# Kernel tuning notes

Measured on AMD Instinct MI355X. Metric: run time of the kernel, lower is better.

Reference implementation:

```python
import jax, jax.numpy as jnp
import numpy as np

B, T, D = 2, 2048, 1024
H = 16
HD = D // H
WINDOW = 128
N_GLOBAL = 1
SCALE = 1.0 / np.sqrt(HD)


def _attend_mask(T):
    # True = allowed to attend: banded local window + global rows/cols
    idx = jnp.arange(T)
    dist = jnp.abs(idx[:, None] - idx[None, :])
    attend = dist <= WINDOW
    glb = idx < N_GLOBAL
    attend = attend | glb[:, None] | glb[None, :]
    return attend  # [T, T] bool


def setup_inputs() -> dict:
    key = jax.random.key(0)
    ks = jax.random.split(key, 5)
    scale_w = 1.0 / np.sqrt(D)
    return {
        "x": jax.random.normal(ks[0], (B, T, D), dtype=jnp.float32),
        "Wq": jax.random.normal(ks[1], (D, D), dtype=jnp.float32) * scale_w,
        "Wk": jax.random.normal(ks[2], (D, D), dtype=jnp.float32) * scale_w,
        "Wv": jax.random.normal(ks[3], (D, D), dtype=jnp.float32) * scale_w,
        "Wo": jax.random.normal(ks[4], (D, D), dtype=jnp.float32) * scale_w,
    }


def reference(x, Wq, Wk, Wv, Wo):
    Bb, Tt, Dd = x.shape
    # torch nn.Linear: y = x @ W.T
    q = (x @ Wq.T).reshape(Bb, Tt, H, HD).transpose(0, 2, 1, 3)  # [B,H,T,hd]
    k = (x @ Wk.T).reshape(Bb, Tt, H, HD).transpose(0, 2, 1, 3)
    v = (x @ Wv.T).reshape(Bb, Tt, H, HD).transpose(0, 2, 1, 3)

    attend = _attend_mask(Tt)  # [T,T]
    logits = jnp.einsum("bhqd,bhkd->bhqk", q, k) * SCALE
    logits = jnp.where(attend[None, None, :, :], logits, -jnp.inf)
    weights = jax.nn.softmax(logits, axis=-1)
    weights = jnp.nan_to_num(weights)
    out = jnp.einsum("bhqk,bhkd->bhqd", weights, v)
    out = out.transpose(0, 2, 1, 3).reshape(Bb, Tt, Dd)
    return out @ Wo.T
```

## Files before the change

kernel.cpp:

```cpp
#include <hip/hip_runtime.h>

typedef unsigned short u16;
typedef __attribute__((ext_vector_type(8))) __bf16 bf16x8;
typedef __attribute__((ext_vector_type(4))) float f32x4;
typedef __attribute__((ext_vector_type(8))) u16 u16x8;

#define T_SEQ 2048
#define DIM   1024
#define HDIM  64
#define WIN   128
#define XN_EL (2 * T_SEQ * DIM)
#define VP    392

#define AS1 __attribute__((address_space(1)))
#define AS3 __attribute__((address_space(3)))

__device__ __forceinline__ u16 f2bf(float f) {
  union { float f; unsigned u; } v; v.f = f;
  unsigned r = v.u + 0x7fffu + ((v.u >> 16) & 1u);
  return (u16)(r >> 16);
}
__device__ __forceinline__ float bf2f(u16 u) {
  union { unsigned u; float f; } v; v.u = ((unsigned)u) << 16; return v.f;
}
__device__ __forceinline__ void bar() {
  asm volatile("" ::: "memory");
  __builtin_amdgcn_s_barrier();
  asm volatile("" ::: "memory");
}

__global__ __launch_bounds__(256) void cvt_all(
    const float* __restrict__ x,  const float* __restrict__ wq,
    const float* __restrict__ wk, const float* __restrict__ wv,
    const float* __restrict__ wo, u16* __restrict__ xb, u16* __restrict__ wb) {
  const int bid = blockIdx.x;
  const float* s;
  u16* d;
  int off;
  if (bid < 2048) {
    s = x; d = xb; off = bid * 2048;
  } else {
    const int w = bid - 2048;
    const int m = w >> 9;
    s = (m == 0) ? wq : ((m == 1) ? wk : ((m == 2) ? wv : wo));
    d = wb + ((size_t)m << 20);
    off = (w & 511) * 2048;
  }
  const int i = off + threadIdx.x * 8;
  const float4* s4 = (const float4*)(s + i);
  float4 a = s4[0], b = s4[1];
  u16x8 r;
  r[0] = f2bf(a.x); r[1] = f2bf(a.y); r[2] = f2bf(a.z); r[3] = f2bf(a.w);
  r[4] = f2bf(b.x); r[5] = f2bf(b.y); r[6] = f2bf(b.z); r[7] = f2bf(b.w);
  *(u16x8*)(d + i) = r;
}

__global__ __launch_bounds__(512, 2) void gemm8(
    const u16* __restrict__ A, const u16* __restrict__ B,
    u16* __restrict__ C, int nbm) {
  constexpr int NT = 16;
  __shared__ u16 As[2][256 * 64];
  __shared__ u16 Bs[2][192 * 64];

  const int tid = threadIdx.x;
  const int lane = tid & 63;
  const int wid = tid >> 6;
  const int wr = wid >> 2, wc = wid & 3;
  const int c15 = lane & 15, g = lane >> 4;
  const int lr = lane >> 3;
  const int lcs = ((lane & 7) ^ lr) << 3;

  const int cpx = gridDim.x >> 3;
  const int bid = ((int)blockIdx.x & 7) * cpx + ((int)blockIdx.x >> 3);
  const int bm = bid % nbm;
  const int nb = bid / nbm;
  const u16* Ab = A + (size_t)bm * 256 * DIM;
  const u16* Bb = B + (size_t)nb * 192 * DIM;

  f32x4 acc[8][3];
#pragma unroll
  for (int m = 0; m < 8; ++m)
#pragma unroll
    for (int n = 0; n < 3; ++n) acc[m][n] = (f32x4){0.f, 0.f, 0.f, 0.f};

  auto stAh = [&](int buf, int half, int t) {
    const int k0 = t * 64;
#pragma unroll
    for (int i = 0; i < 2; ++i) {
      const int c = half * 16 + wid * 2 + i;
      __builtin_amdgcn_global_load_lds(
          (const AS1 void*)(Ab + (size_t)(c * 8 + lr) * DIM + k0 + lcs),
          (AS3 void*)(&As[buf][c * 512]), 16, 0, 0);
    }
  };
  auto stBt = [&](int buf, int third, int t) {
    const int k0 = t * 64;
    const int c = third * 8 + wid;
    __builtin_amdgcn_global_load_lds(
        (const AS1 void*)(Bb + (size_t)(c * 8 + lr) * DIM + k0 + lcs),
        (AS3 void*)(&Bs[buf][c * 512]), 16, 0, 0);
  };

  stAh(0, 0, 0); stAh(0, 1, 0);
  stBt(0, 0, 0); stBt(0, 1, 0); stBt(0, 2, 0);
  stBt(1, 0, 1); stBt(1, 1, 1); stBt(1, 2, 1);
  asm volatile("s_waitcnt vmcnt(3)" ::: "memory");
  bar();

  for (int t2 = 0; t2 < NT; t2 += 2) {
    bf16x8 bfrag[3][2];
#pragma unroll
    for (int p = 0; p < 8; ++p) {
      const int q = p & 3;
      const int buf = (p >> 2);
      if (q == 0) {
#pragma unroll
        for (int n = 0; n < 3; ++n)
#pragma unroll
          for (int ks = 0; ks < 2; ++ks) {
            const int r = wc * 48 + n * 16 + c15;
            bfrag[n][ks] = *(const bf16x8*)(
                &Bs[buf][r * 64 + ((ks * 32 + g * 8) ^ ((r & 7) << 3))]);
          }
      }
      bf16x8 af[2][2];
#pragma unroll
      for (int m = 0; m < 2; ++m)
#pragma unroll
        for (int ks = 0; ks < 2; ++ks) {
          const int r = wr * 128 + (q * 2 + m) * 16 + c15;
          af[m][ks] = *(const bf16x8*)(
              &As[buf][r * 64 + ((ks * 32 + g * 8) ^ ((r & 7) << 3))]);
        }
      const bool s2 = (t2 + 2) < NT;
      const bool s3 = (t2 + 3) < NT;
      if (p == 0) {
        stAh(1, 0, t2 + 1);
      } else if (p == 1) {
        stAh(1, 1, t2 + 1);
        if (s2) stBt(0, 0, t2 + 2);
      } else if (p == 2) {
        if (s2) stBt(0, 1, t2 + 2);
      } else if (p == 3) {
        if (s2) { stBt(0, 2, t2 + 2);
                  asm volatile("s_waitcnt vmcnt(3)" ::: "memory"); }
        else    { asm volatile("s_waitcnt vmcnt(0)" ::: "memory"); }
      } else if (p == 4) {
        if (s2) stAh(0, 0, t2 + 2);
      } else if (p == 5) {
        if (s2) stAh(0, 1, t2 + 2);
        if (s3) stBt(1, 0, t2 + 3);
      } else if (p == 6) {
        if (s3) stBt(1, 1, t2 + 3);
      } else {
        if (s3) { stBt(1, 2, t2 + 3);
                  asm volatile("s_waitcnt vmcnt(3)" ::: "memory"); }
        else if (s2) { asm volatile("s_waitcnt vmcnt(0)" ::: "memory"); }
      }
      bar();
      __builtin_amdgcn_s_setprio(1);
#pragma unroll
      for (int m = 0; m < 2; ++m)
#pragma unroll
        for (int n = 0; n < 3; ++n)
#pragma unroll
          for (int ks = 0; ks < 2; ++ks)
            acc[q * 2 + m][n] = __builtin_amdgcn_mfma_f32_16x16x32_bf16(
                af[m][ks], bfrag[n][ks], acc[q * 2 + m][n], 0, 0, 0);
      __builtin_amdgcn_s_setprio(0);
      bar();
    }
  }

#pragma unroll
  for (int m = 0; m < 8; ++m) {
    const int row0 = bm * 256 + wr * 128 + m * 16 + g * 4;
#pragma unroll
    for (int n = 0; n < 3; ++n) {
      const int col = nb * 192 + wc * 48 + n * 16 + c15;
#pragma unroll
      for (int j = 0; j < 4; ++j) {
        u16* dst = C + (size_t)(col >> 10) * (size_t)XN_EL +
                   (col & 1023) + (size_t)(row0 + j) * DIM;
        *dst = f2bf(acc[m][n][j]);
      }
    }
  }
}

template <int BM, int BN, int WM, int WN, int OS, typename OUT_T>
__global__ __launch_bounds__(WM * WN * 64, 2) void gemm3(
    const u16* __restrict__ A, const u16* __restrict__ B,
    OUT_T* __restrict__ C, int nbm) {
  constexpr int NW = WM * WN;
  constexpr int RM = BM / WM, RN = BN / WN;
  constexpr int MF = RM / 16, NF = RN / 16;
  constexpr int MPH = MF / 4;
  constexpr int NT = DIM / 64;
  constexpr int CA = BM / 8, CB = BN / 8;
  constexpr int ANW = CA / NW;
  constexpr int BNW = CB / NW;

  __shared__ u16 As[2][BM * 64];
  __shared__ u16 Bs[2][BN * 64];

  const int tid = threadIdx.x;
  const int lane = tid & 63;
  const int wid = tid >> 6;
  const int wr = wid / WN, wc = wid % WN;
  const int c15 = lane & 15, g = lane >> 4;
  const int lr = lane >> 3;
  const int lcs = ((lane & 7) ^ lr) << 3;

  const int cpx = gridDim.x >> 3;
  const int bid = ((int)blockIdx.x & 7) * cpx + ((int)blockIdx.x >> 3);
  const int bm = bid % nbm;
  const int nb = bid / nbm;
  const u16* Ab = A + (size_t)bm * BM * DIM;
  const u16* Bb = B + (size_t)nb * BN * DIM;

  f32x4 acc[MF][NF];
#pragma unroll
  for (int m = 0; m < MF; ++m)
#pragma unroll
    for (int n = 0; n < NF; ++n) acc[m][n] = (f32x4){0.f, 0.f, 0.f, 0.f};

  auto stA = [&](int buf, int half, int k0) {
#pragma unroll
    for (int i = 0; i < ANW / 2; ++i) {
      const int c = half * (CA / 2) + wid * (ANW / 2) + i;
      __builtin_amdgcn_global_load_lds(
          (const AS1 void*)(Ab + (size_t)(c * 8 + lr) * DIM + k0 + lcs),
          (AS3 void*)(&As[buf][c * 512]), 16, 0, 0);
    }
  };
  auto stB = [&](int buf, int k0) {
#pragma unroll
    for (int i = 0; i < BNW; ++i) {
      const int c = wid * BNW + i;
      __builtin_amdgcn_global_load_lds(
          (const AS1 void*)(Bb + (size_t)(c * 8 + lr) * DIM + k0 + lcs),
          (AS3 void*)(&Bs[buf][c * 512]), 16, 0, 0);
    }
  };

  stA(0, 0, 0); stA(0, 1, 0);
  stB(0, 0); stB(1, 64);
  asm volatile("s_waitcnt vmcnt(4)" ::: "memory");
  bar();

  for (int t = 0; t < NT; ++t) {
    const int buf = t & 1;
    const int k0 = t * 64;
    bf16x8 bfrag[NF][2];
#pragma unroll
    for (int p = 0; p < 4; ++p) {
      if (p == 0) {
#pragma unroll
        for (int n = 0; n < NF; ++n)
#pragma unroll
          for (int ks = 0; ks < 2; ++ks) {
            const int r = wc * RN + n * 16 + c15;
            bfrag[n][ks] = *(const bf16x8*)(
                &Bs[buf][r * 64 + ((ks * 32 + g * 8) ^ ((r & 7) << 3))]);
          }
      }
      bf16x8 af[MPH][2];
#pragma unroll
      for (int m = 0; m < MPH; ++m)
#pragma unroll
        for (int ks = 0; ks < 2; ++ks) {
          const int r = wr * RM + (p * MPH + m) * 16 + c15;
          af[m][ks] = *(const bf16x8*)(
              &As[buf][r * 64 + ((ks * 32 + g * 8) ^ ((r & 7) << 3))]);
        }
      if (p == 0) {
        if (t + 1 < NT) stA(buf ^ 1, 0, k0 + 64);
      } else if (p == 1) {
        if (t + 1 < NT) stA(buf ^ 1, 1, k0 + 64);
      } else if (p == 2) {
        if (t + 2 < NT) stB(buf, k0 + 128);
      } else {
        if (t < NT - 2) asm volatile("s_waitcnt vmcnt(4)" ::: "memory");
        else            asm volatile("s_waitcnt vmcnt(0)" ::: "memory");
      }
      bar();
      __builtin_amdgcn_s_setprio(1);
#pragma unroll
      for (int m = 0; m < MPH; ++m)
#pragma unroll
        for (int n = 0; n < NF; ++n)
#pragma unroll
          for (int ks = 0; ks < 2; ++ks)
            acc[p * MPH + m][n] = __builtin_amdgcn_mfma_f32_16x16x32_bf16(
                af[m][ks], bfrag[n][ks], acc[p * MPH + m][n], 0, 0, 0);
      __builtin_amdgcn_s_setprio(0);
      bar();
    }
  }

#pragma unroll
  for (int m = 0; m < MF; ++m) {
    const int row0 = bm * BM + wr * RM + m * 16 + g * 4;
#pragma unroll
    for (int n = 0; n < NF; ++n) {
      const int col = nb * BN + wc * RN + n * 16 + c15;
#pragma unroll
      for (int j = 0; j < 4; ++j) {
        const size_t idx = (size_t)(row0 + j) * OS + col;
        if constexpr (sizeof(OUT_T) == 2) C[idx] = f2bf(acc[m][n][j]);
        else C[idx] = acc[m][n][j];
      }
    }
  }
}

__global__ __launch_bounds__(256) void sparse_attn(
    const u16* __restrict__ Q, const u16* __restrict__ K,
    const u16* __restrict__ V, u16* __restrict__ AO) {
  __shared__ u16 Ks[384 * 72];
  __shared__ u16 Vt[64 * VP];
  __shared__ u16 Pl[4][16 * 72];
  __shared__ float Pg[4][32];

  const int tid = threadIdx.x;
  const int lane = tid & 63;
  const int wid = tid >> 6;
  const size_t ha = (size_t)blockIdx.z * T_SEQ * DIM + (size_t)blockIdx.y * HDIM;
  const u16* Qp = Q + ha;
  const u16* Kp = K + ha;
  const u16* Vp = V + ha;

  if (blockIdx.x == 0) {
    float* qs   = (float*)(&Pl[0][0]);
    float* ps   = (float*)Ks;
    float* rbuf = (float*)Vt;
    float* red  = (float*)Pg;

    if (tid < HDIM) qs[tid] = bf2f(Qp[tid]);
    __syncthreads();

    float lsum = 0.f;
#pragma unroll
    for (int j = 0; j < 8; ++j) {
      const int k = tid + 256 * j;
      const u16* kr = Kp + (size_t)k * DIM;
      float acc = 0.f;
#pragma unroll
      for (int d0 = 0; d0 < 8; ++d0) {
        u16x8 kv = *(const u16x8*)(kr + d0 * 8);
#pragma unroll
        for (int e = 0; e < 8; ++e) acc += qs[d0 * 8 + e] * bf2f(kv[e]);
      }
      const float p = __expf(acc * 0.125f);
      ps[k] = p;
      lsum += p;
    }
#pragma unroll
    for (int s = 1; s < 64; s <<= 1) lsum += __shfl_xor(lsum, s);
    if (lane == 0) red[wid] = lsum;
    __syncthreads();
    const float denom = red[0] + red[1] + red[2] + red[3];

    const int kg = tid >> 3, dg = tid & 7;
    float facc[8] = {0.f, 0.f, 0.f, 0.f, 0.f, 0.f, 0.f, 0.f};
#pragma unroll 8
    for (int i = 0; i < 64; ++i) {
      const int k = kg * 64 + i;
      const u16x8 vv = *(const u16x8*)(Vp + (size_t)k * DIM + dg * 8);
      const float p = ps[k];
#pragma unroll
      for (int e = 0; e < 8; ++e) facc[e] += p * bf2f(vv[e]);
    }
#pragma unroll
    for (int e = 0; e < 8; ++e) rbuf[kg * 64 + dg * 8 + e] = facc[e];
    __syncthreads();
    if (tid < HDIM) {
      float tot = 0.f;
#pragma unroll
      for (int k2 = 0; k2 < 32; ++k2) tot += rbuf[k2 * 64 + tid];
      AO[ha + tid] = f2bf(tot / denom);
    }
    return;
  }

  const int c15 = lane & 15;
  const int g = lane >> 4;
  const int q0 = (blockIdx.x - 1) * 128;
  const int qw = q0 + wid * 32;

  bf16x8 qA0, qA1, qB0, qB1;
  {
    const u16* qp = Qp + (size_t)(qw + c15) * DIM + g * 8;
    qA0 = *(const bf16x8*)qp;
    qA1 = *(const bf16x8*)(qp + 32);
    const u16* qp2 = qp + 16 * DIM;
    qB0 = *(const bf16x8*)qp2;
    qB1 = *(const bf16x8*)(qp2 + 32);
  }

  const int klo = (q0 > WIN) ? (q0 - WIN) : 0;
  int khi = q0 + 128 + WIN;
  if (khi > T_SEQ) khi = T_SEQ;
  const int nt = (khi - klo) >> 6;

  {
    const int srr = tid >> 2;
    const int scc = (tid & 3) * 16;
    const int vsw = srr ^ (scc & 48);
    const u16* kb = Kp + (size_t)(klo + srr) * DIM + scc;
    const u16* vb = Vp + (size_t)(klo + srr) * DIM + scc;
    u16x8 k0 = *(const u16x8*)kb, k1 = *(const u16x8*)(kb + 8);
    u16x8 v0 = *(const u16x8*)vb, v1 = *(const u16x8*)(vb + 8);
    for (int tt = 0; tt < nt; ++tt) {
      u16x8 ck0 = k0, ck1 = k1, cv0 = v0, cv1 = v1;
      if (tt + 1 < nt) {
        const u16* kn = kb + (size_t)(tt + 1) * 64 * DIM;
        const u16* vn = vb + (size_t)(tt + 1) * 64 * DIM;
        k0 = *(const u16x8*)kn; k1 = *(const u16x8*)(kn + 8);
        v0 = *(const u16x8*)vn; v1 = *(const u16x8*)(vn + 8);
      }
      const int lr = tt * 64 + srr;
      *(u16x8*)(Ks + lr * 72 + scc) = ck0;
      *(u16x8*)(Ks + lr * 72 + scc + 8) = ck1;
      const int vc = tt * 64 + vsw;
#pragma unroll
      for (int e = 0; e < 8; ++e) {
        Vt[(scc + e) * VP + vc] = cv0[e];
        Vt[(scc + 8 + e) * VP + vc] = cv1[e];
      }
    }
  }
  __syncthreads();

  float lrA[4] = {0.f, 0.f, 0.f, 0.f}, lrB[4] = {0.f, 0.f, 0.f, 0.f};
  f32x4 aoA[4], aoB[4];
#pragma unroll
  for (int c = 0; c < 4; ++c) {
    aoA[c] = (f32x4){0.f, 0.f, 0.f, 0.f};
    aoB[c] = (f32x4){0.f, 0.f, 0.f, 0.f};
  }

  for (int ti = 0; ti < nt; ++ti) {
    const int kt = klo + ti * 64;
    const int tb = ti * 64;

    auto do_group = [&](const bf16x8& qf0, const bf16x8& qf1, int r0,
                        float* lrun, f32x4* ao) {
      f32x4 s[4];
#pragma unroll
      for (int t = 0; t < 4; ++t) {
        const u16* kr = Ks + (size_t)(tb + t * 16 + c15) * 72 + g * 8;
        bf16x8 ka = *(const bf16x8*)kr;
        bf16x8 kb2 = *(const bf16x8*)(kr + 32);
        f32x4 z = (f32x4){0.f, 0.f, 0.f, 0.f};
        z = __builtin_amdgcn_mfma_f32_16x16x32_bf16(qf0, ka, z, 0, 0, 0);
        s[t] = __builtin_amdgcn_mfma_f32_16x16x32_bf16(qf1, kb2, z, 0, 0, 0);
      }
      if (kt >= r0 - 113 && kt <= r0 + 65) {
#pragma unroll
        for (int j = 0; j < 4; ++j) {
#pragma unroll
          for (int t = 0; t < 4; ++t) {
            const float p = __expf(s[t][j] * 0.125f);
            lrun[j] += p;
            Pl[wid][(g * 4 + j) * 72 + t * 16 + c15] = f2bf(p);
          }
        }
      } else {
#pragma unroll
        for (int j = 0; j < 4; ++j) {
          const int qg = r0 + g * 4 + j;
#pragma unroll
          for (int t = 0; t < 4; ++t) {
            const int kg = kt + t * 16 + c15;
            const int dd = qg - kg;
            const bool ok = (kg == 0) || (dd <= WIN && dd >= -WIN);
            const float p = ok ? __expf(s[t][j] * 0.125f) : 0.f;
            lrun[j] += p;
            Pl[wid][(g * 4 + j) * 72 + t * 16 + c15] = f2bf(p);
          }
        }
      }
      asm volatile("s_waitcnt lgkmcnt(0)" ::: "memory");

      const bf16x8 pa0 = *(const bf16x8*)(&Pl[wid][c15 * 72 + g * 8]);
      const bf16x8 pa1 = *(const bf16x8*)(&Pl[wid][c15 * 72 + 32 + g * 8]);
#pragma unroll
      for (int c = 0; c < 4; ++c) {
        const int rb = (c * 16 + c15) * VP;
        bf16x8 va = *(const bf16x8*)(Vt + rb + tb + ((g * 8) ^ (c << 4)));
        bf16x8 vb2 = *(const bf16x8*)(Vt + rb + tb + ((32 + g * 8) ^ (c << 4)));
        ao[c] = __builtin_amdgcn_mfma_f32_16x16x32_bf16(pa0, va, ao[c], 0, 0, 0);
        ao[c] = __builtin_amdgcn_mfma_f32_16x16x32_bf16(pa1, vb2, ao[c], 0, 0, 0);
      }
    };

    do_group(qA0, qA1, qw, lrA, aoA);
    do_group(qB0, qB1, qw + 16, lrB, aoB);
  }

  float ltA[4], ltB[4];
#pragma unroll
  for (int j = 0; j < 4; ++j) {
    float a = lrA[j], b = lrB[j];
    a += __shfl_xor(a, 1); b += __shfl_xor(b, 1);
    a += __shfl_xor(a, 2); b += __shfl_xor(b, 2);
    a += __shfl_xor(a, 4); b += __shfl_xor(b, 4);
    a += __shfl_xor(a, 8); b += __shfl_xor(b, 8);
    ltA[j] = a; ltB[j] = b;
  }

  if (klo > 0) {
    const u16x8 k0a = *(const u16x8*)(Kp + g * 8);
    const u16x8 k0b = *(const u16x8*)(Kp + 32 + g * 8);
    const u16x8 qa0 = *(const u16x8*)&qA0;
    const u16x8 qa1 = *(const u16x8*)&qA1;
    const u16x8 qb0 = *(const u16x8*)&qB0;
    const u16x8 qb1 = *(const u16x8*)&qB1;
    float sgA = 0.f, sgB = 0.f;
#pragma unroll
    for (int e = 0; e < 8; ++e) {
      sgA += bf2f(qa0[e]) * bf2f(k0a[e]) + bf2f(qa1[e]) * bf2f(k0b[e]);
      sgB += bf2f(qb0[e]) * bf2f(k0a[e]) + bf2f(qb1[e]) * bf2f(k0b[e]);
    }
    sgA += __shfl_xor(sgA, 16); sgA += __shfl_xor(sgA, 32);
    sgB += __shfl_xor(sgB, 16); sgB += __shfl_xor(sgB, 32);
    Pg[wid][c15] = __expf(sgA * 0.125f);
    Pg[wid][16 + c15] = __expf(sgB * 0.125f);
    asm volatile("s_waitcnt lgkmcnt(0)" ::: "memory");
#pragma unroll
    for (int j = 0; j < 4; ++j) {
      const float pA = Pg[wid][g * 4 + j];
      const float pB = Pg[wid][16 + g * 4 + j];
      ltA[j] += pA;
      ltB[j] += pB;
#pragma unroll
      for (int c = 0; c < 4; ++c) {
        const float v0 = bf2f(Vp[c * 16 + c15]);
        aoA[c][j] += pA * v0;
        aoB[c][j] += pB * v0;
      }
    }
  }

#pragma unroll
  for (int j = 0; j < 4; ++j) {
    const int qrA = qw + g * 4 + j;
    const int qrB = qrA + 16;
    const float invA = 1.0f / ltA[j];
    const float invB = 1.0f / ltB[j];
#pragma unroll
    for (int c = 0; c < 4; ++c) {
      if (qrA != 0)
        AO[ha + (size_t)qrA * DIM + c * 16 + c15] = f2bf(aoA[c][j] * invA);
      AO[ha + (size_t)qrB * DIM + c * 16 + c15] = f2bf(aoB[c][j] * invB);
    }
  }
}

extern "C" void kernel_launch(void* const* d_in, const int* in_sizes, int n_in,
                              void* d_out, int out_size, void* d_ws, size_t ws_size,
                              hipStream_t stream) {
  const float* x  = (const float*)d_in[0];
  const float* Wq = (const float*)d_in[1];
  const float* Wk = (const float*)d_in[2];
  const float* Wv = (const float*)d_in[3];
  const float* Wo = (const float*)d_in[4];
  float* out = (float*)d_out;

  const int WN = DIM * DIM;

  u16* ws  = (u16*)d_ws;
  u16* xb  = ws;
  u16* wb  = ws + (size_t)XN_EL;
  u16* Wob = wb + (size_t)3 * WN;
  u16* Qb  = wb + (size_t)4 * WN;
  u16* Kb  = Qb + (size_t)XN_EL;
  u16* Vb  = Kb + (size_t)XN_EL;

  cvt_all<<<4096, 256, 0, stream>>>(x, Wq, Wk, Wv, Wo, xb, wb);

  gemm8<<<256, 512, 0, stream>>>(xb, wb, Qb, 16);

  sparse_attn<<<dim3(17, 16, 2), 256, 0, stream>>>(Qb, Kb, Vb, xb);

  gemm3<128, 128, 2, 2, DIM, float><<<256, 256, 0, stream>>>(xb, Wob, out, 32);
}
```

Baseline: 108.8 us.

## Store V transposed from QKV GEMM and pipeline attention K/V tiles via LDS DMA

The QKV GEMM epilogue now writes V in a per-head transposed [d][T] layout with packed 4-element stores. The attention kernel uses this to replace its up-front register-staged K/V load and LDS transpose with a 3-stage ring buffer filled by global_load_lds, using XOR swizzling so reads avoid bank conflicts. This overlaps the K/V fetch with MFMA work and shrinks LDS use. The global-row block also reads the transposed V along contiguous rows. The cost is more complex vmcnt and barrier bookkeeping, and a transposed write pattern in the GEMM epilogue.

```diff
diff --git a/kernel.cpp b/kernel.cpp
--- a/kernel.cpp
+++ b/kernel.cpp
@@ -4,13 +4,13 @@
 typedef __attribute__((ext_vector_type(8))) __bf16 bf16x8;
 typedef __attribute__((ext_vector_type(4))) float f32x4;
 typedef __attribute__((ext_vector_type(8))) u16 u16x8;
+typedef __attribute__((ext_vector_type(4))) u16 u16x4;
 
 #define T_SEQ 2048
 #define DIM   1024
 #define HDIM  64
 #define WIN   128
 #define XN_EL (2 * T_SEQ * DIM)
-#define VP    392
 
 #define AS1 __attribute__((address_space(1)))
 #define AS3 __attribute__((address_space(3)))
@@ -178,11 +178,21 @@
 #pragma unroll
     for (int n = 0; n < 3; ++n) {
       const int col = nb * 192 + wc * 48 + n * 16 + c15;
-#pragma unroll
-      for (int j = 0; j < 4; ++j) {
-        u16* dst = C + (size_t)(col >> 10) * (size_t)XN_EL +
-                   (col & 1023) + (size_t)(row0 + j) * DIM;
-        *dst = f2bf(acc[m][n][j]);
+      if (col < 2048) {
+#pragma unroll
+        for (int j = 0; j < 4; ++j) {
+          u16* dst = C + (size_t)(col >> 10) * (size_t)XN_EL +
+                     (col & 1023) + (size_t)(row0 + j) * DIM;
+          *dst = f2bf(acc[m][n][j]);
+        }
+      } else {
+        const int h = (col - 2048) >> 6, dd = (col - 2048) & 63;
+        u16x4 pk;
+#pragma unroll
+        for (int j = 0; j < 4; ++j) pk[j] = f2bf(acc[m][n][j]);
+        const size_t vidx =
+            ((size_t)((row0 >> 11) * 16 + h) * 64 + dd) * T_SEQ + (row0 & 2047);
+        *(u16x4*)(C + (size_t)2 * XN_EL + vidx) = pk;
       }
     }
   }
@@ -317,9 +327,9 @@
 
 __global__ __launch_bounds__(256) void sparse_attn(
     const u16* __restrict__ Q, const u16* __restrict__ K,
-    const u16* __restrict__ V, u16* __restrict__ AO) {
-  __shared__ u16 Ks[384 * 72];
-  __shared__ u16 Vt[64 * VP];
+    const u16* __restrict__ VT, u16* __restrict__ AO) {
+  __shared__ u16 Ks[3][64 * 64];
+  __shared__ u16 Vs[3][64 * 64];
   __shared__ u16 Pl[4][16 * 72];
   __shared__ float Pg[4][32];
 
@@ -327,14 +337,15 @@
   const int lane = tid & 63;
   const int wid = tid >> 6;
   const size_t ha = (size_t)blockIdx.z * T_SEQ * DIM + (size_t)blockIdx.y * HDIM;
+  const size_t hv = ((size_t)blockIdx.z * 16 + blockIdx.y) * HDIM * T_SEQ;
   const u16* Qp = Q + ha;
   const u16* Kp = K + ha;
-  const u16* Vp = V + ha;
+  const u16* Vp = VT + hv;
 
   if (blockIdx.x == 0) {
     float* qs   = (float*)(&Pl[0][0]);
-    float* ps   = (float*)Ks;
-    float* rbuf = (float*)Vt;
+    float* ps   = (float*)(&Ks[0][0]);
+    float* rbuf = (float*)(&Vs[0][0]);
     float* red  = (float*)Pg;
 
     if (tid < HDIM) qs[tid] = bf2f(Qp[tid]);
@@ -362,23 +373,19 @@
     __syncthreads();
     const float denom = red[0] + red[1] + red[2] + red[3];
 
-    const int kg = tid >> 3, dg = tid & 7;
-    float facc[8] = {0.f, 0.f, 0.f, 0.f, 0.f, 0.f, 0.f, 0.f};
-#pragma unroll 8
-    for (int i = 0; i < 64; ++i) {
-      const int k = kg * 64 + i;
-      const u16x8 vv = *(const u16x8*)(Vp + (size_t)k * DIM + dg * 8);
-      const float p = ps[k];
-#pragma unroll
-      for (int e = 0; e < 8; ++e) facc[e] += p * bf2f(vv[e]);
-    }
-#pragma unroll
-    for (int e = 0; e < 8; ++e) rbuf[kg * 64 + dg * 8 + e] = facc[e];
+    const int d = tid & 63, kc = tid >> 6;
+    const u16* vr = Vp + (size_t)d * T_SEQ + kc * 512;
+    float facc = 0.f;
+#pragma unroll 4
+    for (int i = 0; i < 512; i += 8) {
+      const u16x8 vv = *(const u16x8*)(vr + i);
+#pragma unroll
+      for (int e = 0; e < 8; ++e) facc += ps[kc * 512 + i + e] * bf2f(vv[e]);
+    }
+    rbuf[kc * 64 + d] = facc;
     __syncthreads();
     if (tid < HDIM) {
-      float tot = 0.f;
-#pragma unroll
-      for (int k2 = 0; k2 < 32; ++k2) tot += rbuf[k2 * 64 + tid];
+      const float tot = rbuf[tid] + rbuf[64 + tid] + rbuf[128 + tid] + rbuf[192 + tid];
       AO[ha + tid] = f2bf(tot / denom);
     }
     return;
@@ -399,60 +406,56 @@
     qB1 = *(const bf16x8*)(qp2 + 32);
   }
 
+  float lrA[4] = {0.f, 0.f, 0.f, 0.f}, lrB[4] = {0.f, 0.f, 0.f, 0.f};
+  f32x4 aoA[4], aoB[4];
+#pragma unroll
+  for (int c = 0; c < 4; ++c) {
+    aoA[c] = (f32x4){0.f, 0.f, 0.f, 0.f};
+    aoB[c] = (f32x4){0.f, 0.f, 0.f, 0.f};
+  }
+
   const int klo = (q0 > WIN) ? (q0 - WIN) : 0;
   int khi = q0 + 128 + WIN;
   if (khi > T_SEQ) khi = T_SEQ;
   const int nt = (khi - klo) >> 6;
 
-  {
-    const int srr = tid >> 2;
-    const int scc = (tid & 3) * 16;
-    const int vsw = srr ^ (scc & 48);
-    const u16* kb = Kp + (size_t)(klo + srr) * DIM + scc;
-    const u16* vb = Vp + (size_t)(klo + srr) * DIM + scc;
-    u16x8 k0 = *(const u16x8*)kb, k1 = *(const u16x8*)(kb + 8);
-    u16x8 v0 = *(const u16x8*)vb, v1 = *(const u16x8*)(vb + 8);
-    for (int tt = 0; tt < nt; ++tt) {
-      u16x8 ck0 = k0, ck1 = k1, cv0 = v0, cv1 = v1;
-      if (tt + 1 < nt) {
-        const u16* kn = kb + (size_t)(tt + 1) * 64 * DIM;
-        const u16* vn = vb + (size_t)(tt + 1) * 64 * DIM;
-        k0 = *(const u16x8*)kn; k1 = *(const u16x8*)(kn + 8);
-        v0 = *(const u16x8*)vn; v1 = *(const u16x8*)(vn + 8);
-      }
-      const int lr = tt * 64 + srr;
-      *(u16x8*)(Ks + lr * 72 + scc) = ck0;
-      *(u16x8*)(Ks + lr * 72 + scc + 8) = ck1;
-      const int vc = tt * 64 + vsw;
-#pragma unroll
-      for (int e = 0; e < 8; ++e) {
-        Vt[(scc + e) * VP + vc] = cv0[e];
-        Vt[(scc + 8 + e) * VP + vc] = cv1[e];
-      }
-    }
-  }
-  __syncthreads();
-
-  float lrA[4] = {0.f, 0.f, 0.f, 0.f}, lrB[4] = {0.f, 0.f, 0.f, 0.f};
-  f32x4 aoA[4], aoB[4];
-#pragma unroll
-  for (int c = 0; c < 4; ++c) {
-    aoA[c] = (f32x4){0.f, 0.f, 0.f, 0.f};
-    aoB[c] = (f32x4){0.f, 0.f, 0.f, 0.f};
-  }
+  const int lr = lane >> 3;
+  const int lcs = ((lane & 7) ^ lr) << 3;
+
+  auto stage = [&](int buf, int ti2) {
+    const int kt = klo + ti2 * 64;
+#pragma unroll
+    for (int i = 0; i < 2; ++i) {
+      const int c = wid * 2 + i;
+      __builtin_amdgcn_global_load_lds(
+          (const AS1 void*)(Kp + (size_t)(kt + c * 8 + lr) * DIM + lcs),
+          (AS3 void*)(&Ks[buf][c * 512]), 16, 0, 0);
+      __builtin_amdgcn_global_load_lds(
+          (const AS1 void*)(Vp + (size_t)(c * 8 + lr) * T_SEQ + kt + lcs),
+          (AS3 void*)(&Vs[buf][c * 512]), 16, 0, 0);
+    }
+  };
+
+  stage(0, 0);
+  stage(1, 1);
+  asm volatile("s_waitcnt vmcnt(4)" ::: "memory");
+  bar();
 
   for (int ti = 0; ti < nt; ++ti) {
     const int kt = klo + ti * 64;
-    const int tb = ti * 64;
+    const int buf = ti % 3;
+    if (ti + 2 < nt) stage((ti + 2) % 3, ti + 2);
 
     auto do_group = [&](const bf16x8& qf0, const bf16x8& qf1, int r0,
                         float* lrun, f32x4* ao) {
       f32x4 s[4];
 #pragma unroll
       for (int t = 0; t < 4; ++t) {
-        const u16* kr = Ks + (size_t)(tb + t * 16 + c15) * 72 + g * 8;
-        bf16x8 ka = *(const bf16x8*)kr;
-        bf16x8 kb2 = *(const bf16x8*)(kr + 32);
+        const int r = t * 16 + c15;
+        bf16x8 ka = *(const bf16x8*)(
+            &Ks[buf][r * 64 + ((g * 8) ^ ((r & 7) << 3))]);
+        bf16x8 kb2 = *(const bf16x8*)(
+            &Ks[buf][r * 64 + ((32 + g * 8) ^ ((r & 7) << 3))]);
         f32x4 z = (f32x4){0.f, 0.f, 0.f, 0.f};
         z = __builtin_amdgcn_mfma_f32_16x16x32_bf16(qf0, ka, z, 0, 0, 0);
         s[t] = __builtin_amdgcn_mfma_f32_16x16x32_bf16(qf1, kb2, z, 0, 0, 0);
@@ -488,9 +491,11 @@
       const bf16x8 pa1 = *(const bf16x8*)(&Pl[wid][c15 * 72 + 32 + g * 8]);
 #pragma unroll
       for (int c = 0; c < 4; ++c) {
-        const int rb = (c * 16 + c15) * VP;
-        bf16x8 va = *(const bf16x8*)(Vt + rb + tb + ((g * 8) ^ (c << 4)));
-        bf16x8 vb2 = *(const bf16x8*)(Vt + rb + tb + ((32 + g * 8) ^ (c << 4)));
+        const int r = c * 16 + c15;
+        bf16x8 va = *(const bf16x8*)(
+            &Vs[buf][r * 64 + ((g * 8) ^ ((r & 7) << 3))]);
+        bf16x8 vb2 = *(const bf16x8*)(
+            &Vs[buf][r * 64 + ((32 + g * 8) ^ ((r & 7) << 3))]);
         ao[c] = __builtin_amdgcn_mfma_f32_16x16x32_bf16(pa0, va, ao[c], 0, 0, 0);
         ao[c] = __builtin_amdgcn_mfma_f32_16x16x32_bf16(pa1, vb2, ao[c], 0, 0, 0);
       }
@@ -498,6 +503,10 @@
 
     do_group(qA0, qA1, qw, lrA, aoA);
     do_group(qB0, qB1, qw + 16, lrB, aoB);
+
+    if (ti + 2 < nt)      asm volatile("s_waitcnt vmcnt(4)" ::: "memory");
+    else if (ti + 1 < nt) asm volatile("s_waitcnt vmcnt(0)" ::: "memory");
+    if (ti + 1 < nt) bar();
   }
 
   float ltA[4], ltB[4];
@@ -537,7 +546,7 @@
       ltB[j] += pB;
 #pragma unroll
       for (int c = 0; c < 4; ++c) {
-        const float v0 = bf2f(Vp[c * 16 + c15]);
+        const float v0 = bf2f(Vp[(size_t)(c * 16 + c15) * T_SEQ]);
         aoA[c][j] += pA * v0;
         aoB[c][j] += pB * v0;
       }
@@ -577,13 +586,13 @@
   u16* Wob = wb + (size_t)3 * WN;
   u16* Qb  = wb + (size_t)4 * WN;
   u16* Kb  = Qb + (size_t)XN_EL;
-  u16* Vb  = Kb + (size_t)XN_EL;
+  u16* VTb = Qb + (size_t)2 * XN_EL;
 
   cvt_all<<<4096, 256, 0, stream>>>(x, Wq, Wk, Wv, Wo, xb, wb);
 
   gemm8<<<256, 512, 0, stream>>>(xb, wb, Qb, 16);
 
-  sparse_attn<<<dim3(17, 16, 2), 256, 0, stream>>>(Qb, Kb, Vb, xb);
+  sparse_attn<<<dim3(17, 16, 2), 256, 0, stream>>>(Qb, Kb, VTb, xb);
 
   gemm3<128, 128, 2, 2, DIM, float><<<256, 256, 0, stream>>>(xb, Wob, out, 32);
 }
```

After: 113.7 us. 1.05x slower.
